# Performance work log

Hardware: AMD Instinct MI355X
Metric: run time of the kernel (lower is better)

The kernel has to match this reference:

```python
import jax, jax.numpy as jnp
import numpy as np

NBITS = 1
GROUP_SIZE = 64
OUT_F = 4096
IN_F = 4096


def setup_inputs() -> dict:
    key = jax.random.key(0)
    k1, k2, k3, k4, k5 = jax.random.split(key, 5)
    x = jax.random.normal(k1, (8192, IN_F), dtype=jnp.float32)
    # packed 1-bit weights: 8 bits per byte, stored as int32 in [0,256)
    W_packed = jax.random.randint(k2, (OUT_F, IN_F // 8), 0, 256, dtype=jnp.int32)
    n_groups = OUT_F * IN_F // GROUP_SIZE
    scale = jax.random.uniform(k3, (n_groups, 1), dtype=jnp.float32) * 0.02 + 0.005
    zero = jax.random.normal(k4, (n_groups, 1), dtype=jnp.float32) * 0.5
    bias = jax.random.normal(k5, (OUT_F,), dtype=jnp.float32) * 0.02
    return {"x": x, "W_packed": W_packed, "scale": scale, "zero": zero, "bias": bias}


def _unpack_1bit(W_packed):
    # (out, in//8) int -> (out, in) float bits, bit 0 first within each byte
    bits = (W_packed[..., None] >> jnp.arange(8, dtype=jnp.int32)) & 1  # (out, in//8, 8)
    return bits.reshape(W_packed.shape[0], -1).astype(jnp.float32)      # (out, in)


def _dequantise(W_packed, scale, zero):
    W_q = _unpack_1bit(W_packed)                       # (out, in)
    W_grouped = W_q.reshape(-1, GROUP_SIZE)            # (n_groups, group_size), axis=1 grouping
    W_hat = (W_grouped - zero) * scale                 # per-group affine dequant
    return W_hat.reshape(OUT_F, IN_F)


def reference(x, W_packed, scale, zero, bias):
    W_hat = _dequantise(W_packed, scale, zero)
    # F.linear: x @ W_hat.T + bias
    return jnp.dot(x, W_hat.T) + bias
```

## Files before the change

### kernel.cpp

```cpp
#include <hip/hip_runtime.h>
#include <hip/hip_bf16.h>

#define IN_F   4096
#define OUT_F  4096

typedef __bf16 bf16;
typedef __attribute__((ext_vector_type(8)))  __bf16 bf16x8;
typedef __attribute__((ext_vector_type(4)))  __bf16 bf16x4;
typedef __attribute__((ext_vector_type(4)))  float  floatx4;
typedef __attribute__((ext_vector_type(16))) float  floatx16;

__global__ __launch_bounds__(256) void prep_kernel(
    const float* __restrict__ x,  bf16* __restrict__ xb,
    const int* __restrict__ Wp,   const float* __restrict__ scale,
    const float* __restrict__ zero, bf16* __restrict__ Wb, int nxb)
{
    if ((int)blockIdx.x < nxb) {
        const size_t i = (size_t)blockIdx.x * 256 + threadIdx.x;
        float4 v = ((const float4*)x)[i];
        bf16x4 b = { (bf16)v.x, (bf16)v.y, (bf16)v.z, (bf16)v.w };
        ((bf16x4*)xb)[i] = b;
    } else {
        const int tid = (blockIdx.x - nxb) * 256 + threadIdx.x;
        const int n = tid >> 9;
        const int b = tid & 511;
        const int g = (n << 6) + (b >> 3);
        const float sc = scale[g];
        const float zp = zero[g];
        const bf16 hi = (bf16)((1.0f - zp) * sc);
        const bf16 lo = (bf16)((0.0f - zp) * sc);
        const int v = Wp[tid];
        bf16x8 w;
#pragma unroll
        for (int j = 0; j < 8; ++j) w[j] = ((v >> j) & 1) ? hi : lo;
        *(bf16x8*)&Wb[(size_t)tid * 8] = w;
    }
}

__device__ __forceinline__ void gload_lds16(const void* g, void* l) {
    __builtin_amdgcn_global_load_lds(
        (const __attribute__((address_space(1))) unsigned int*)g,
        (__attribute__((address_space(3))) unsigned int*)l, 16, 0, 0);
}

__global__ __launch_bounds__(256) void bf16_gemm_bt_kernel(
    const bf16* __restrict__ A,
    const bf16* __restrict__ B,
    const float* __restrict__ bias,
    float* __restrict__ out)
{
    __shared__ __align__(16) bf16 as[128 * 64];
    __shared__ __align__(16) bf16 bs[128 * 64];

    const int t      = threadIdx.x;
    const int lane   = t & 63;
    const int wave   = t >> 6;
    const int lane32 = lane & 31;
    const int half   = lane >> 5;
    const int wm     = wave >> 1;
    const int wn     = wave & 1;

    const int n0 = blockIdx.x * 128;
    const int m0 = blockIdx.y * 128;

    floatx16 acc[2][2];
#pragma unroll
    for (int i = 0; i < 2; ++i)
#pragma unroll
        for (int j = 0; j < 2; ++j)
#pragma unroll
            for (int r = 0; r < 16; ++r) acc[i][j][r] = 0.f;

    const int srow8 = lane >> 3;
    const int sunit = lane & 7;

    for (int kt = 0; kt < IN_F / 64; ++kt) {
#pragma unroll
        for (int i = 0; i < 4; ++i) {
            const int row   = wave * 32 + i * 8 + srow8;
            const int gunit = sunit ^ (row & 7);
            gload_lds16(A + (size_t)(m0 + row) * IN_F + kt * 64 + gunit * 8,
                        &as[(wave * 32 + i * 8) * 64]);
            gload_lds16(B + (size_t)(n0 + row) * IN_F + kt * 64 + gunit * 8,
                        &bs[(wave * 32 + i * 8) * 64]);
        }
        __syncthreads();

#pragma unroll
        for (int s = 0; s < 4; ++s) {
            const int u = s * 2 + half;
            bf16x8 af[2], bfr[2];
#pragma unroll
            for (int i = 0; i < 2; ++i) {
                const int r = wm * 64 + i * 32 + lane32;
                af[i] = *(const bf16x8*)&as[r * 64 + (u ^ (r & 7)) * 8];
            }
#pragma unroll
            for (int j = 0; j < 2; ++j) {
                const int r = wn * 64 + j * 32 + lane32;
                bfr[j] = *(const bf16x8*)&bs[r * 64 + (u ^ (r & 7)) * 8];
            }
#pragma unroll
            for (int i = 0; i < 2; ++i)
#pragma unroll
                for (int j = 0; j < 2; ++j)
                    acc[i][j] = __builtin_amdgcn_mfma_f32_32x32x16_bf16(
                        af[i], bfr[j], acc[i][j], 0, 0, 0);
        }
        __syncthreads();
    }

#pragma unroll
    for (int j = 0; j < 2; ++j) {
        const int col = n0 + wn * 64 + j * 32 + lane32;
        const float bv = bias[col];
#pragma unroll
        for (int i = 0; i < 2; ++i) {
            const int rowbase = m0 + wm * 64 + i * 32 + 4 * half;
#pragma unroll
            for (int reg = 0; reg < 16; ++reg) {
                const int row = rowbase + (reg & 3) + 8 * (reg >> 2);
                out[(size_t)row * OUT_F + col] = acc[i][j][reg] + bv;
            }
        }
    }
}

#define SA 72
#define SB 72
__global__ __launch_bounds__(256) void hqq_gemm_fused_kernel(
    const float* __restrict__ x, const int* __restrict__ Wp,
    const float* __restrict__ scale, const float* __restrict__ zero,
    const float* __restrict__ bias, float* __restrict__ out)
{
    __shared__ __align__(16) bf16 asmem[128 * SA];
    __shared__ __align__(16) bf16 bsmem[128 * SB];
    const int t = threadIdx.x, lane = t & 63, wave = t >> 6;
    const int lane16 = lane & 15, kq = lane >> 4;
    const int wm = wave >> 1, wn = wave & 1;
    const int n0 = blockIdx.x * 128, m0 = blockIdx.y * 128;
    floatx4 acc[4][4];
#pragma unroll
    for (int i = 0; i < 4; ++i)
#pragma unroll
        for (int j = 0; j < 4; ++j) acc[i][j] = (floatx4){0.f, 0.f, 0.f, 0.f};
    const int a_col4 = t & 15, a_row0 = t >> 4;
    const int b_nl = t >> 1, b_half = t & 1;
    for (int kt = 0; kt < IN_F / 64; ++kt) {
        const float* xp = x + (size_t)(m0 + a_row0) * IN_F + kt * 64 + a_col4 * 4;
#pragma unroll
        for (int p = 0; p < 8; ++p) {
            float4 v = *(const float4*)(xp + (size_t)(p * 16) * IN_F);
            bf16x4 b = { (bf16)v.x, (bf16)v.y, (bf16)v.z, (bf16)v.w };
            *(bf16x4*)&asmem[(a_row0 + p * 16) * SA + a_col4 * 4] = b;
        }
        {
            const int4 v = *(const int4*)(Wp + (size_t)(n0 + b_nl) * (IN_F / 8)
                                          + kt * 8 + b_half * 4);
            const int g = (n0 + b_nl) * (IN_F / 64) + kt;
            const float sc = scale[g], zp = zero[g];
            const bf16 hi = (bf16)((1.0f - zp) * sc), lo = (bf16)(0.0f - zp * sc);
            const int vals[4] = {v.x, v.y, v.z, v.w};
#pragma unroll
            for (int e = 0; e < 4; ++e) {
                bf16x8 w;
#pragma unroll
                for (int j = 0; j < 8; ++j) w[j] = ((vals[e] >> j) & 1) ? hi : lo;
                *(bf16x8*)&bsmem[b_nl * SB + b_half * 32 + e * 8] = w;
            }
        }
        __syncthreads();
#pragma unroll
        for (int ks = 0; ks < 2; ++ks) {
            bf16x8 af[4], bfr[4];
#pragma unroll
            for (int i = 0; i < 4; ++i)
                af[i] = *(const bf16x8*)&asmem[(wm * 64 + i * 16 + lane16) * SA + ks * 32 + kq * 8];
#pragma unroll
            for (int j = 0; j < 4; ++j)
                bfr[j] = *(const bf16x8*)&bsmem[(wn * 64 + j * 16 + lane16) * SB + ks * 32 + kq * 8];
#pragma unroll
            for (int i = 0; i < 4; ++i)
#pragma unroll
                for (int j = 0; j < 4; ++j)
                    acc[i][j] = __builtin_amdgcn_mfma_f32_16x16x32_bf16(af[i], bfr[j], acc[i][j], 0, 0, 0);
        }
        __syncthreads();
    }
#pragma unroll
    for (int j = 0; j < 4; ++j) {
        const int col = n0 + wn * 64 + j * 16 + lane16;
        const float bv = bias[col];
#pragma unroll
        for (int i = 0; i < 4; ++i) {
            const int row = m0 + wm * 64 + i * 16 + kq * 4;
#pragma unroll
            for (int r = 0; r < 4; ++r)
                out[(size_t)(row + r) * OUT_F + col] = acc[i][j][r] + bv;
        }
    }
}

extern "C" void kernel_launch(void* const* d_in, const int* in_sizes, int n_in,
                              void* d_out, int out_size, void* d_ws, size_t ws_size,
                              hipStream_t stream) {
    const float* x     = (const float*)d_in[0];
    const int*   Wp    = (const int*)d_in[1];
    const float* scale = (const float*)d_in[2];
    const float* zero  = (const float*)d_in[3];
    const float* bias  = (const float*)d_in[4];
    float*       out   = (float*)d_out;

    const int M = in_sizes[0] / IN_F;
    const size_t need = (size_t)M * IN_F * 2 + (size_t)OUT_F * IN_F * 2;

    if (ws_size >= need) {
        bf16* xb = (bf16*)d_ws;
        bf16* Wb = (bf16*)((char*)d_ws + (size_t)M * IN_F * 2);

        const int nxb = (M * IN_F / 4) / 256;
        const int nwb = (OUT_F * IN_F / 8) / 256;
        prep_kernel<<<nxb + nwb, 256, 0, stream>>>(x, xb, Wp, scale, zero, Wb, nxb);

        dim3 grid(OUT_F / 128, M / 128);
        bf16_gemm_bt_kernel<<<grid, 256, 0, stream>>>(xb, Wb, bias, out);
    } else {
        dim3 grid(OUT_F / 128, M / 128);
        hqq_gemm_fused_kernel<<<grid, 256, 0, stream>>>(x, Wp, scale, zero, bias, out);
    }
}
```

Before: 507.6 us.

## Replace bf16 GEMM with 256x256 double-buffered 8-phase pipelined kernel

Swaps the 128x128 single-buffered bf16 GEMM for a 256x256-tile, 512-thread kernel. It double-buffers LDS and interleaves async global-to-LDS staging of the next K tile with four MFMA phases per tile, using explicit barriers, waitcnts and setprio. It also remaps workgroup IDs for XCD-aware scheduling and widens the x-to-bf16 conversion to 8 elements per thread. The intent is to hide global load latency behind MFMA work and raise arithmetic intensity per tile. The cost is higher register and LDS pressure (128KB LDS) and fragile hand-tuned vmcnt accounting.

```diff
diff --git a/kernel.cpp b/kernel.cpp
--- a/kernel.cpp
+++ b/kernel.cpp
@@ -3,12 +3,13 @@
 
 #define IN_F   4096
 #define OUT_F  4096
+#define BK     64
+#define NTILES (IN_F / BK)
 
 typedef __bf16 bf16;
 typedef __attribute__((ext_vector_type(8)))  __bf16 bf16x8;
 typedef __attribute__((ext_vector_type(4)))  __bf16 bf16x4;
 typedef __attribute__((ext_vector_type(4)))  float  floatx4;
-typedef __attribute__((ext_vector_type(16))) float  floatx16;
 
 __global__ __launch_bounds__(256) void prep_kernel(
     const float* __restrict__ x,  bf16* __restrict__ xb,
@@ -17,9 +18,12 @@
 {
     if ((int)blockIdx.x < nxb) {
         const size_t i = (size_t)blockIdx.x * 256 + threadIdx.x;
-        float4 v = ((const float4*)x)[i];
-        bf16x4 b = { (bf16)v.x, (bf16)v.y, (bf16)v.z, (bf16)v.w };
-        ((bf16x4*)xb)[i] = b;
+        const float4 v0 = ((const float4*)x)[2 * i];
+        const float4 v1 = ((const float4*)x)[2 * i + 1];
+        bf16x8 b;
+        b[0] = (bf16)v0.x; b[1] = (bf16)v0.y; b[2] = (bf16)v0.z; b[3] = (bf16)v0.w;
+        b[4] = (bf16)v1.x; b[5] = (bf16)v1.y; b[6] = (bf16)v1.z; b[7] = (bf16)v1.w;
+        ((bf16x8*)xb)[i] = b;
     } else {
         const int tid = (blockIdx.x - nxb) * 256 + threadIdx.x;
         const int n = tid >> 9;
@@ -43,85 +47,140 @@
         (__attribute__((address_space(3))) unsigned int*)l, 16, 0, 0);
 }
 
-__global__ __launch_bounds__(256) void bf16_gemm_bt_kernel(
+#define CFENCE asm volatile("" ::: "memory")
+#define SBAR() do { CFENCE; __builtin_amdgcn_s_barrier(); CFENCE; } while (0)
+#define WAIT_LGKM0 asm volatile("s_waitcnt lgkmcnt(0)" ::: "memory")
+
+#define STAGE(src, ldsTile, q, row0, kti) do {                                 \
+    const int r_  = (q) * 64 + wave * 8 + srow;                                \
+    const int gu_ = sun ^ (r_ & 7);                                            \
+    gload_lds16((src) + (size_t)((row0) + r_) * IN_F + (kti) * BK + gu_ * 8,   \
+                (ldsTile) + ((q) * 64 + wave * 8) * BK);                       \
+} while (0)
+
+#define LDFRAG(tile, row, u) \
+    (*(const bf16x8*)((tile) + (row) * BK + (((u) ^ ((row) & 7)) << 3)))
+
+#define LOAD_A(tile, MS)                                                       \
+    _Pragma("unroll")                                                          \
+    for (int i = 0; i < 4; ++i)                                                \
+        _Pragma("unroll")                                                      \
+        for (int ks = 0; ks < 2; ++ks)                                         \
+            af[i][ks] = LDFRAG((tile), wm * 128 + (MS) * 64 + i * 16 + l15,    \
+                               ks * 4 + l4);
+
+#define LOAD_B(tile, NS)                                                       \
+    _Pragma("unroll")                                                          \
+    for (int j = 0; j < 2; ++j)                                                \
+        _Pragma("unroll")                                                      \
+        for (int ks = 0; ks < 2; ++ks)                                         \
+            bfr[j][ks] = LDFRAG((tile), wn * 64 + (NS) * 32 + j * 16 + l15,    \
+                                ks * 4 + l4);
+
+#define MFMA_QUAD(AI, BJ)                                                      \
+    __builtin_amdgcn_s_setprio(1);                                             \
+    _Pragma("unroll")                                                          \
+    for (int i = 0; i < 4; ++i)                                                \
+        _Pragma("unroll")                                                      \
+        for (int j = 0; j < 2; ++j)                                            \
+            _Pragma("unroll")                                                  \
+            for (int ks = 0; ks < 2; ++ks)                                     \
+                acc[(AI) + i][(BJ) + j] =                                      \
+                    __builtin_amdgcn_mfma_f32_16x16x32_bf16(                   \
+                        af[i][ks], bfr[j][ks], acc[(AI) + i][(BJ) + j], 0, 0, 0); \
+    __builtin_amdgcn_s_setprio(0);
+
+__global__ __launch_bounds__(512, 2) void gemm256_8phase_kernel(
     const bf16* __restrict__ A,
     const bf16* __restrict__ B,
     const float* __restrict__ bias,
     float* __restrict__ out)
 {
-    __shared__ __align__(16) bf16 as[128 * 64];
-    __shared__ __align__(16) bf16 bs[128 * 64];
-
-    const int t      = threadIdx.x;
-    const int lane   = t & 63;
-    const int wave   = t >> 6;
-    const int lane32 = lane & 31;
-    const int half   = lane >> 5;
-    const int wm     = wave >> 1;
-    const int wn     = wave & 1;
-
-    const int n0 = blockIdx.x * 128;
-    const int m0 = blockIdx.y * 128;
-
-    floatx16 acc[2][2];
-#pragma unroll
-    for (int i = 0; i < 2; ++i)
-#pragma unroll
-        for (int j = 0; j < 2; ++j)
-#pragma unroll
-            for (int r = 0; r < 16; ++r) acc[i][j][r] = 0.f;
-
-    const int srow8 = lane >> 3;
-    const int sunit = lane & 7;
-
-    for (int kt = 0; kt < IN_F / 64; ++kt) {
-#pragma unroll
-        for (int i = 0; i < 4; ++i) {
-            const int row   = wave * 32 + i * 8 + srow8;
-            const int gunit = sunit ^ (row & 7);
-            gload_lds16(A + (size_t)(m0 + row) * IN_F + kt * 64 + gunit * 8,
-                        &as[(wave * 32 + i * 8) * 64]);
-            gload_lds16(B + (size_t)(n0 + row) * IN_F + kt * 64 + gunit * 8,
-                        &bs[(wave * 32 + i * 8) * 64]);
-        }
-        __syncthreads();
-
-#pragma unroll
-        for (int s = 0; s < 4; ++s) {
-            const int u = s * 2 + half;
-            bf16x8 af[2], bfr[2];
-#pragma unroll
-            for (int i = 0; i < 2; ++i) {
-                const int r = wm * 64 + i * 32 + lane32;
-                af[i] = *(const bf16x8*)&as[r * 64 + (u ^ (r & 7)) * 8];
-            }
-#pragma unroll
-            for (int j = 0; j < 2; ++j) {
-                const int r = wn * 64 + j * 32 + lane32;
-                bfr[j] = *(const bf16x8*)&bs[r * 64 + (u ^ (r & 7)) * 8];
-            }
-#pragma unroll
-            for (int i = 0; i < 2; ++i)
-#pragma unroll
-                for (int j = 0; j < 2; ++j)
-                    acc[i][j] = __builtin_amdgcn_mfma_f32_32x32x16_bf16(
-                        af[i], bfr[j], acc[i][j], 0, 0, 0);
-        }
-        __syncthreads();
-    }
-
-#pragma unroll
-    for (int j = 0; j < 2; ++j) {
-        const int col = n0 + wn * 64 + j * 32 + lane32;
+    __shared__ __align__(16) bf16 as_[2][256 * BK];
+    __shared__ __align__(16) bf16 bs_[2][256 * BK];
+
+    const int t    = threadIdx.x;
+    const int lane = t & 63;
+    const int wave = t >> 6;
+    const int wm   = wave >> 2;
+    const int wn   = wave & 3;
+    const int l15  = lane & 15;
+    const int l4   = lane >> 4;
+    const int srow = lane >> 3;
+    const int sun  = lane & 7;
+
+    const int nwg = (int)gridDim.x;
+    const int cpx = nwg >> 3;
+    const int wg  = ((int)blockIdx.x & 7) * cpx + ((int)blockIdx.x >> 3);
+    const int n0  = (wg & 15) * 256;
+    const int m0  = (wg >> 4) * 256;
+
+    floatx4 acc[8][4];
+#pragma unroll
+    for (int f = 0; f < 8; ++f)
+#pragma unroll
+        for (int g = 0; g < 4; ++g) acc[f][g] = (floatx4){0.f, 0.f, 0.f, 0.f};
+
+#pragma unroll
+    for (int q = 0; q < 4; ++q) STAGE(A, &as_[0][0], q, m0, 0);
+#pragma unroll
+    for (int q = 0; q < 4; ++q) STAGE(B, &bs_[0][0], q, n0, 0);
+    STAGE(A, &as_[1][0], 0, m0, 1);
+    STAGE(A, &as_[1][0], 2, m0, 1);
+    asm volatile("s_waitcnt vmcnt(2)" ::: "memory");
+    SBAR();
+
+    bf16x8 af[4][2], bfr[2][2];
+
+    for (int kt = 0; kt < NTILES; ++kt) {
+        bf16* const At = &as_[kt & 1][0];
+        bf16* const Bt = &bs_[kt & 1][0];
+        bf16* const An = &as_[(kt & 1) ^ 1][0];
+        bf16* const Bn = &bs_[(kt & 1) ^ 1][0];
+        const int s1 = (kt + 1 < NTILES);
+        const int s2 = (kt + 2 < NTILES);
+
+        LOAD_A(At, 0);
+        LOAD_B(Bt, 0);
+        if (s1) { STAGE(B, Bn, 0, n0, kt + 1); STAGE(B, Bn, 1, n0, kt + 1); }
+        SBAR(); WAIT_LGKM0;
+        MFMA_QUAD(0, 0);
+        SBAR();
+
+        LOAD_B(Bt, 1);
+        if (s1) { STAGE(B, Bn, 2, n0, kt + 1); STAGE(B, Bn, 3, n0, kt + 1); }
+        SBAR(); WAIT_LGKM0;
+        MFMA_QUAD(0, 2);
+        if (s1) { asm volatile("s_waitcnt vmcnt(6)" ::: "memory"); }
+        else    { asm volatile("s_waitcnt vmcnt(0)" ::: "memory"); }
+        SBAR();
+
+        LOAD_A(At, 1);
+        LOAD_B(Bt, 0);
+        if (s1) { STAGE(A, An, 1, m0, kt + 1); STAGE(A, An, 3, m0, kt + 1); }
+        SBAR(); WAIT_LGKM0;
+        MFMA_QUAD(4, 0);
+        SBAR();
+
+        LOAD_B(Bt, 1);
+        if (s2) { STAGE(A, At, 0, m0, kt + 2); STAGE(A, At, 2, m0, kt + 2); }
+        SBAR(); WAIT_LGKM0;
+        MFMA_QUAD(4, 2);
+        if (s2) { asm volatile("s_waitcnt vmcnt(4)" ::: "memory"); }
+        else    { asm volatile("s_waitcnt vmcnt(2)" ::: "memory"); }
+        SBAR();
+    }
+
+#pragma unroll
+    for (int g = 0; g < 4; ++g) {
+        const int col = n0 + wn * 64 + g * 16 + l15;
         const float bv = bias[col];
 #pragma unroll
-        for (int i = 0; i < 2; ++i) {
-            const int rowbase = m0 + wm * 64 + i * 32 + 4 * half;
-#pragma unroll
-            for (int reg = 0; reg < 16; ++reg) {
-                const int row = rowbase + (reg & 3) + 8 * (reg >> 2);
-                out[(size_t)row * OUT_F + col] = acc[i][j][reg] + bv;
-            }
+        for (int f = 0; f < 8; ++f) {
+            const int row = m0 + wm * 128 + f * 16 + l4 * 4;
+#pragma unroll
+            for (int r = 0; r < 4; ++r)
+                out[(size_t)(row + r) * OUT_F + col] = acc[f][g][r] + bv;
         }
     }
 }
@@ -214,16 +273,16 @@
     const int M = in_sizes[0] / IN_F;
     const size_t need = (size_t)M * IN_F * 2 + (size_t)OUT_F * IN_F * 2;
 
-    if (ws_size >= need) {
+    if (ws_size >= need && (M % 256) == 0) {
         bf16* xb = (bf16*)d_ws;
         bf16* Wb = (bf16*)((char*)d_ws + (size_t)M * IN_F * 2);
 
-        const int nxb = (M * IN_F / 4) / 256;
+        const int nxb = (M * IN_F / 8) / 256;
         const int nwb = (OUT_F * IN_F / 8) / 256;
         prep_kernel<<<nxb + nwb, 256, 0, stream>>>(x, xb, Wp, scale, zero, Wb, nxb);
 
-        dim3 grid(OUT_F / 128, M / 128);
-        bf16_gemm_bt_kernel<<<grid, 256, 0, stream>>>(xb, Wb, bias, out);
+        gemm256_8phase_kernel<<<dim3((OUT_F / 256) * (M / 256)), 512, 0, stream>>>(
+            xb, Wb, bias, out);
     } else {
         dim3 grid(OUT_F / 128, M / 128);
         hqq_gemm_fused_kernel<<<grid, 256, 0, stream>>>(x, Wp, scale, zero, bias, out);
```

New measurement: 484.3 us. 4.6% less time.
